# Kernel optimization log

Measured on AMD Instinct MI355X. Metric: run time of the kernel, lower is better.

Reference implementation:

```python
import jax, jax.numpy as jnp
import numpy as np

NU, NI, E, DIN, D, NB, NC = 100000, 50000, 2000000, 64, 64, 2, 5


def setup_inputs() -> dict:
    key = jax.random.key(0)
    ks = jax.random.split(key, 10)
    return {
        "ufeat": jax.random.normal(ks[0], (NU, DIN), dtype=jnp.float32),
        "ifeat": jax.random.normal(ks[1], (NI, DIN), dtype=jnp.float32),
        "c_u": jax.random.uniform(ks[2], (NU, 1), dtype=jnp.float32),
        "c_i": jax.random.uniform(ks[3], (NI, 1), dtype=jnp.float32),
        "W_user": jax.random.normal(ks[4], (DIN, D), dtype=jnp.float32) * (1.0 / np.sqrt(DIN)),
        "W_item": jax.random.normal(ks[5], (DIN, D), dtype=jnp.float32) * (1.0 / np.sqrt(DIN)),
        "P": jax.random.normal(ks[6], (NB, D, D), dtype=jnp.float32) * (1.0 / np.sqrt(D)),
        "Wc": jax.random.normal(ks[7], (NC, NB), dtype=jnp.float32),
        "src": jax.random.randint(ks[8], (E,), 0, NU, dtype=jnp.int32),
        "dst": jax.random.randint(ks[9], (E,), 0, NI, dtype=jnp.int32),
    }


def reference(ufeat, ifeat, c_u, c_i, W_user, W_item, P, Wc, src, dst):
    # --- GCMCGraphConv user->item: feat @ W, scale by c_j, copy_u + sum scatter, scale by c_i ---
    msg_u = (ufeat @ W_user) * c_u                                   # [NU, D]
    h_item = jax.ops.segment_sum(msg_u[src], dst, num_segments=ifeat.shape[0]) * c_i  # [NI, D]
    # --- GCMCGraphConv item->user (reverse edges) ---
    msg_i = (ifeat @ W_item) * c_i                                   # [NI, D]
    h_user = jax.ops.segment_sum(msg_i[dst], src, num_segments=ufeat.shape[0]) * c_u  # [NU, D]
    # --- BiDecoder: per-edge bilinear dot for each basis, then basis combine ---
    hu_b = jnp.einsum('nd,sde->nse', h_user, P)                      # [NU, NB, D]
    sr = jnp.einsum('esd,ed->es', hu_b[src], h_item[dst])            # [E, NB]
    out = sr @ Wc.T                                                  # [E, NC]
    return out
```

## Files before the change

### kernel.cpp

```cpp
#include <hip/hip_runtime.h>
#include <hip/hip_fp16.h>

#define NUu 100000
#define NIi 50000
#define NEe 2000000

#define NCBI   25
#define NCBU   49
#define NCB    74
#define NBLK1  512
#define CHUNK1 ((NEe + NBLK1 - 1) / NBLK1)

#define BR    16
#define NBKI  3125
#define NBKU  6250
#define CAPI  896
#define CAPU  512
#define FSUB2 8
#define FOWN2 16
#define FPC   128

__global__ __launch_bounds__(256) void gemm64_both(
    const float* __restrict__ ufeat, const float* __restrict__ ifeat,
    const float* __restrict__ W_user, const float* __restrict__ W_item,
    const float* __restrict__ c_u, const float* __restrict__ c_i,
    __half* __restrict__ msg_u, __half* __restrict__ msg_i)
{
    __shared__ float Wl[64 * 64];
    __shared__ float rows[16][64];
    const int tid  = threadIdx.x;
    const int user = (blockIdx.x < (NUu + 15) / 16) ? 1 : 0;
    const int bid  = user ? blockIdx.x : blockIdx.x - (NUu + 15) / 16;
    const float* feat = user ? ufeat : ifeat;
    const float* W    = user ? W_user : W_item;
    const float* cvec = user ? c_u : c_i;
    __half* out       = user ? msg_u : msg_i;
    const int N       = user ? NUu : NIi;

    for (int i = tid; i < 4096; i += 256) Wl[i] = W[i];
    const int r0 = bid * 16;
    for (int i = tid; i < 16 * 64; i += 256) {
        int r = r0 + (i >> 6);
        rows[i >> 6][i & 63] = (r < N) ? feat[(size_t)r * 64 + (i & 63)] : 0.f;
    }
    __syncthreads();
    const int col = tid & 63;
    const int rq  = tid >> 6;
    for (int rr = rq; rr < 16; rr += 4) {
        int r = r0 + rr;
        if (r >= N) continue;
        float s = 0.f;
        #pragma unroll
        for (int k = 0; k < 64; ++k)
            s = fmaf(rows[rr][k], Wl[k * 64 + col], s);
        out[(size_t)r * 64 + col] = __float2half(s * cvec[r]);
    }
}

__global__ __launch_bounds__(256) void hist1(
    const int* __restrict__ src, const int* __restrict__ dst, int* __restrict__ counts)
{
    __shared__ int cnt[NCB];
    const int tid = threadIdx.x;
    if (tid < NCB) cnt[tid] = 0;
    __syncthreads();
    const int beg = blockIdx.x * CHUNK1;
    const int end = min(NEe, beg + CHUNK1);
    for (int t = beg + tid; t < end; t += 256) {
        int s = src[t], d = dst[t];
        atomicAdd(&cnt[d >> 11], 1);
        atomicAdd(&cnt[NCBI + (s >> 11)], 1);
    }
    __syncthreads();
    if (tid < NCB) counts[tid * NBLK1 + blockIdx.x] = cnt[tid];
}

__global__ __launch_bounds__(256) void scan1(
    const int* __restrict__ counts, int* __restrict__ slotbase, int* __restrict__ rowptrC)
{
    __shared__ int tot[NCB], base[NCB];
    const int tid = threadIdx.x;
    if (tid < NCB) {
        int s = 0;
        for (int b = 0; b < NBLK1; ++b) s += counts[tid * NBLK1 + b];
        tot[tid] = s;
    }
    __syncthreads();
    if (tid == 0) {
        int run = 0;
        for (int c = 0; c < NCB; ++c) { base[c] = run; rowptrC[c] = run; run += tot[c]; }
        rowptrC[NCB] = run;
    }
    __syncthreads();
    if (tid < NCB) {
        int run = base[tid];
        for (int b = 0; b < NBLK1; ++b) {
            slotbase[tid * NBLK1 + b] = run;
            run += counts[tid * NBLK1 + b];
        }
    }
}

__global__ __launch_bounds__(256) void fill1(
    const int* __restrict__ src, const int* __restrict__ dst,
    const int* __restrict__ slotbase, unsigned int* __restrict__ payC)
{
    __shared__ int cur[NCB];
    const int tid = threadIdx.x;
    if (tid < NCB) cur[tid] = slotbase[tid * NBLK1 + blockIdx.x];
    __syncthreads();
    const int beg = blockIdx.x * CHUNK1;
    const int end = min(NEe, beg + CHUNK1);
    for (int t = beg + tid; t < end; t += 256) {
        int s = src[t], d = dst[t];
        int p1 = atomicAdd(&cur[d >> 11], 1);
        payC[p1] = ((unsigned)(d & 2047) << 17) | (unsigned)s;
        int p2 = atomicAdd(&cur[NCBI + (s >> 11)], 1);
        payC[p2] = ((unsigned)(s & 2047) << 16) | (unsigned)d;
    }
}

__global__ __launch_bounds__(256) void fine_split2(
    const unsigned int* __restrict__ payC, const int* __restrict__ rowptrC,
    unsigned int* __restrict__ payI, int* __restrict__ cntFI,
    unsigned int* __restrict__ payU, int* __restrict__ cntFU)
{
    __shared__ int cur[FOWN2];
    const int tid = threadIdx.x;
    int bid = blockIdx.x;
    const int user = (bid >= NCBI * FSUB2) ? 1 : 0;
    if (user) bid -= NCBI * FSUB2;
    const int cbl = bid / FSUB2;
    const int sub = bid % FSUB2;
    const int c   = user ? (NCBI + cbl) : cbl;
    const int CAP = user ? CAPU : CAPI;
    unsigned int* __restrict__ payF = user ? payU : payI;
    int*          __restrict__ cntF = user ? cntFU : cntFI;

    if (tid < FOWN2) cur[tid] = 0;
    __syncthreads();

    const int beg = rowptrC[c], end = rowptrC[c + 1];
    const int a    = min(end, beg + ((4 - (beg & 3)) & 3));
    const int vend = a + ((end - a) & ~3);

#define FS_PROC(u)                                                          \
    {                                                                       \
        unsigned int _u = (u);                                              \
        int lr  = user ? (int)(_u >> 16) : (int)(_u >> 17);                 \
        int fbl = lr >> 4;                                                  \
        if ((fbl >> 4) == sub) {                                            \
            int pos = atomicAdd(&cur[fbl & 15], 1);                         \
            if (pos < CAP) {                                                \
                unsigned int g = user ? (_u & 0xffffu) : (_u & 0x1ffffu);   \
                payF[(size_t)(cbl * FPC + fbl) * CAP + pos] =               \
                    ((unsigned)(lr & 15) << 17) | g;                        \
            }                                                               \
        }                                                                   \
    }

    if (tid < a - beg) FS_PROC(payC[beg + tid]);
    for (int i = a + tid * 4; i < vend; i += 1024) {
        uint4 v = *(const uint4*)(payC + i);
        FS_PROC(v.x); FS_PROC(v.y); FS_PROC(v.z); FS_PROC(v.w);
    }
    {
        int i = vend + tid;
        if (i < end) FS_PROC(payC[i]);
    }
#undef FS_PROC

    __syncthreads();
    if (tid < FOWN2)
        cntF[cbl * FPC + sub * FOWN2 + tid] = min(cur[tid], CAP);
}

__global__ __launch_bounds__(256) void seg_both(
    const unsigned int* __restrict__ payI, const int* __restrict__ cntFI,
    const __half* __restrict__ msg_u, const float* __restrict__ c_i,
    __half2* __restrict__ h_item,
    const unsigned int* __restrict__ payU, const int* __restrict__ cntFU,
    const __half* __restrict__ msg_i, const float* __restrict__ c_u,
    __half2* __restrict__ h_user)
{
    __shared__ unsigned int sorted[CAPI];
    __shared__ float acc[BR * 64];
    __shared__ int cnt16[BR];
    __shared__ int base16[BR];
    const int tid  = threadIdx.x;
    const int user = (blockIdx.x >= NBKI) ? 1 : 0;
    const int buk  = user ? (blockIdx.x - NBKI) : blockIdx.x;
    const int CAP  = user ? CAPU : CAPI;
    const int len  = min((user ? cntFU : cntFI)[buk], CAP);
    const unsigned int* bp = (user ? payU : payI) + (size_t)buk * CAP;
    const __half* msg      = user ? msg_i : msg_u;
    const float* cvec      = user ? c_u : c_i;
    __half2* hout          = user ? h_user : h_item;
    const int N            = user ? NUu : NIi;

    for (int i = tid; i < BR * 64; i += 256) acc[i] = 0.f;
    if (tid < BR) cnt16[tid] = 0;
    __syncthreads();
    for (int i = tid; i < len; i += 256)
        atomicAdd(&cnt16[bp[i] >> 17], 1);
    __syncthreads();
    if (tid == 0) {
        int run = 0;
        #pragma unroll
        for (int r = 0; r < BR; ++r) { base16[r] = run; run += cnt16[r]; }
    }
    __syncthreads();
    if (tid < BR) cnt16[tid] = base16[tid];
    __syncthreads();
    for (int i = tid; i < len; i += 256) {
        unsigned int p = bp[i];
        int pos = atomicAdd(&cnt16[p >> 17], 1);
        sorted[pos] = p;
    }
    __syncthreads();

    const int lane  = tid & 63;
    const int wv    = tid >> 6;
    const int chunk = (len + 3) >> 2;
    const int lo = wv * chunk;
    const int hi = min(lo + chunk, len);
    float facc = 0.f;
    int crow = -1;
    for (int i = lo; i < hi; i += 8) {
        unsigned int pk[8];
        float vk[8];
        #pragma unroll
        for (int k = 0; k < 8; ++k)
            pk[k] = sorted[min(i + k, hi - 1)];
        #pragma unroll
        for (int k = 0; k < 8; ++k)
            vk[k] = __half2float(msg[(size_t)(pk[k] & 0x1ffffu) * 64 + lane]);
        #pragma unroll
        for (int k = 0; k < 8; ++k) {
            if (i + k < hi) {
                int r = (int)(pk[k] >> 17);
                if (r != crow) {
                    if (crow >= 0) atomicAdd(&acc[crow * 64 + lane], facc);
                    crow = r;
                    facc = 0.f;
                }
                facc += vk[k];
            }
        }
    }
    if (crow >= 0) atomicAdd(&acc[crow * 64 + lane], facc);
    __syncthreads();

    const int r0 = buk * BR;
    for (int idx = tid; idx < BR * 32; idx += 256) {
        int r = idx >> 5, j2 = idx & 31;
        int R = r0 + r;
        if (R < N) {
            float c = cvec[R];
            hout[(size_t)R * 32 + j2] =
                __floats2half2_rn(acc[r * 64 + 2 * j2] * c, acc[r * 64 + 2 * j2 + 1] * c);
        }
    }
}

__global__ __launch_bounds__(256) void basis_projT_h(
    const __half* __restrict__ h, const float* __restrict__ P,
    __half* __restrict__ hb, int N)
{
    __shared__ float Pl[2 * 64 * 65];
    __shared__ float rows[8][64];
    const int tid = threadIdx.x;
    for (int i = tid; i < 8192; i += 256) {
        int b = i >> 12, rem = i & 4095, dg = rem >> 6, kg = rem & 63;
        Pl[b * 4160 + kg * 65 + dg] = P[i];
    }
    const int r0 = blockIdx.x * 8;
    for (int i = tid; i < 512; i += 256) {
        int r = r0 + (i >> 6);
        rows[i >> 6][i & 63] = (r < N) ? __half2float(h[(size_t)r * 64 + (i & 63)]) : 0.f;
    }
    __syncthreads();
    const int col = tid & 63;
    const int b   = (tid >> 6) & 1;
    const int rh  = tid >> 7;
    for (int rr = rh; rr < 8; rr += 2) {
        int r = r0 + rr;
        if (r >= N) continue;
        float s = 0.f;
        #pragma unroll
        for (int k = 0; k < 64; ++k)
            s = fmaf(rows[rr][k], Pl[b * 4160 + k * 65 + col], s);
        hb[((size_t)r * 2 + b) * 64 + col] = __float2half(s);
    }
}

__global__ __launch_bounds__(256) void edge_out_h(
    const uint4* __restrict__ hu,
    const uint4* __restrict__ hib,
    const int* __restrict__ src, const int* __restrict__ dst,
    const float* __restrict__ Wc, float* __restrict__ out, int nocts)
{
    const int l   = threadIdx.x & 63;
    const int q   = l >> 3;
    const int j   = l & 7;
    const int wid = blockIdx.x * 4 + (threadIdx.x >> 6);
    const int nw  = gridDim.x * 4;
    const float wcA = (j < 5) ? Wc[2 * j]     : 0.f;
    const float wcB = (j < 5) ? Wc[2 * j + 1] : 0.f;
    for (int t = wid; t < nocts; t += nw) {
        int e = t * 8 + q;
        int s = src[e], d = dst[e];
        uint4 ua = hu[(size_t)s * 8 + j];
        uint4 b0 = hib[(size_t)d * 16 + j];
        uint4 b1 = hib[(size_t)d * 16 + 8 + j];
        float2 u0 = __half22float2(*(const __half2*)&ua.x);
        float2 u1 = __half22float2(*(const __half2*)&ua.y);
        float2 u2 = __half22float2(*(const __half2*)&ua.z);
        float2 u3 = __half22float2(*(const __half2*)&ua.w);
        float2 v0 = __half22float2(*(const __half2*)&b0.x);
        float2 v1 = __half22float2(*(const __half2*)&b0.y);
        float2 v2 = __half22float2(*(const __half2*)&b0.z);
        float2 v3 = __half22float2(*(const __half2*)&b0.w);
        float2 w0 = __half22float2(*(const __half2*)&b1.x);
        float2 w1 = __half22float2(*(const __half2*)&b1.y);
        float2 w2 = __half22float2(*(const __half2*)&b1.z);
        float2 w3 = __half22float2(*(const __half2*)&b1.w);
        float p0 = u0.x * v0.x + u0.y * v0.y + u1.x * v1.x + u1.y * v1.y
                 + u2.x * v2.x + u2.y * v2.y + u3.x * v3.x + u3.y * v3.y;
        float p1 = u0.x * w0.x + u0.y * w0.y + u1.x * w1.x + u1.y * w1.y
                 + u2.x * w2.x + u2.y * w2.y + u3.x * w3.x + u3.y * w3.y;
        #pragma unroll
        for (int m = 1; m < 8; m <<= 1) {
            p0 += __shfl_xor(p0, m, 64);
            p1 += __shfl_xor(p1, m, 64);
        }
        if (j < 5) out[(size_t)e * 5 + j] = p0 * wcA + p1 * wcB;
    }
}

extern "C" void kernel_launch(void* const* d_in, const int* in_sizes, int n_in,
                              void* d_out, int out_size, void* d_ws, size_t ws_size,
                              hipStream_t stream) {
    const float* ufeat  = (const float*)d_in[0];
    const float* ifeat  = (const float*)d_in[1];
    const float* c_u    = (const float*)d_in[2];
    const float* c_i    = (const float*)d_in[3];
    const float* W_user = (const float*)d_in[4];
    const float* W_item = (const float*)d_in[5];
    const float* P      = (const float*)d_in[6];
    const float* Wc     = (const float*)d_in[7];
    const int*   src    = (const int*)d_in[8];
    const int*   dst    = (const int*)d_in[9];
    float* out = (float*)d_out;
    char*  ws  = (char*)d_ws;

    __half*       msg_u    = (__half*)(ws);
    __half*       msg_i    = (__half*)(ws + 12800000);
    __half*       h_item   = (__half*)(ws + 19200000);
    __half*       h_user   = (__half*)(ws + 25600000);
    unsigned int* payC     = (unsigned int*)(ws + 38400000);
    __half*       hi_b     = (__half*)(ws + 38400000);
    unsigned int* payI     = (unsigned int*)(ws + 54400000);
    unsigned int* payU     = (unsigned int*)(ws + 65600000);
    int*          counts   = (int*)(ws + 78400000);
    int*          slotbase = (int*)(ws + 78551552);
    int*          rowptrC  = (int*)(ws + 78703104);
    int*          cntFI    = (int*)(ws + 78703404);
    int*          cntFU    = (int*)(ws + 78716204);

    gemm64_both<<<(NUu + 15) / 16 + (NIi + 15) / 16, 256, 0, stream>>>(
        ufeat, ifeat, W_user, W_item, c_u, c_i, msg_u, msg_i);

    hist1<<<NBLK1, 256, 0, stream>>>(src, dst, counts);
    scan1<<<1, 256, 0, stream>>>(counts, slotbase, rowptrC);
    fill1<<<NBLK1, 256, 0, stream>>>(src, dst, slotbase, payC);
    fine_split2<<<(NCBI + NCBU) * FSUB2, 256, 0, stream>>>(
        payC, rowptrC, payI, cntFI, payU, cntFU);

    seg_both<<<NBKI + NBKU, 256, 0, stream>>>(
        payI, cntFI, msg_u, c_i, (__half2*)h_item,
        payU, cntFU, msg_i, c_u, (__half2*)h_user);

    basis_projT_h<<<(NIi + 7) / 8, 256, 0, stream>>>(h_item, P, hi_b, NIi);
    edge_out_h<<<2048, 256, 0, stream>>>(
        (const uint4*)h_user, (const uint4*)hi_b, src, dst, Wc, out, NEe / 8);
}
```

Baseline: 425.7 us.

## Vectorize edge binning loads and split segment gather into half2 half-waves

```diff
diff --git a/kernel.cpp b/kernel.cpp
--- a/kernel.cpp
+++ b/kernel.cpp
@@ -8,8 +8,8 @@
 #define NCBI   25
 #define NCBU   49
 #define NCB    74
-#define NBLK1  512
-#define CHUNK1 ((NEe + NBLK1 - 1) / NBLK1)
+#define NBLK1  500
+#define CHUNK1 4000
 
 #define BR    16
 #define NBKI  3125
@@ -65,11 +65,17 @@
     if (tid < NCB) cnt[tid] = 0;
     __syncthreads();
     const int beg = blockIdx.x * CHUNK1;
-    const int end = min(NEe, beg + CHUNK1);
-    for (int t = beg + tid; t < end; t += 256) {
-        int s = src[t], d = dst[t];
-        atomicAdd(&cnt[d >> 11], 1);
-        atomicAdd(&cnt[NCBI + (s >> 11)], 1);
+    for (int i = beg + tid * 4; i < beg + CHUNK1; i += 1024) {
+        uint4 s4 = *(const uint4*)(src + i);
+        uint4 d4 = *(const uint4*)(dst + i);
+        atomicAdd(&cnt[d4.x >> 11], 1);
+        atomicAdd(&cnt[d4.y >> 11], 1);
+        atomicAdd(&cnt[d4.z >> 11], 1);
+        atomicAdd(&cnt[d4.w >> 11], 1);
+        atomicAdd(&cnt[NCBI + (s4.x >> 11)], 1);
+        atomicAdd(&cnt[NCBI + (s4.y >> 11)], 1);
+        atomicAdd(&cnt[NCBI + (s4.z >> 11)], 1);
+        atomicAdd(&cnt[NCBI + (s4.w >> 11)], 1);
     }
     __syncthreads();
     if (tid < NCB) counts[tid * NBLK1 + blockIdx.x] = cnt[tid];
@@ -110,14 +116,23 @@
     if (tid < NCB) cur[tid] = slotbase[tid * NBLK1 + blockIdx.x];
     __syncthreads();
     const int beg = blockIdx.x * CHUNK1;
-    const int end = min(NEe, beg + CHUNK1);
-    for (int t = beg + tid; t < end; t += 256) {
-        int s = src[t], d = dst[t];
-        int p1 = atomicAdd(&cur[d >> 11], 1);
-        payC[p1] = ((unsigned)(d & 2047) << 17) | (unsigned)s;
-        int p2 = atomicAdd(&cur[NCBI + (s >> 11)], 1);
-        payC[p2] = ((unsigned)(s & 2047) << 16) | (unsigned)d;
-    }
+#define F1_PROC(ss, dd)                                                     \
+    {                                                                       \
+        int _s = (int)(ss), _d = (int)(dd);                                 \
+        int p1 = atomicAdd(&cur[_d >> 11], 1);                              \
+        payC[p1] = ((unsigned)(_d & 2047) << 17) | (unsigned)_s;            \
+        int p2 = atomicAdd(&cur[NCBI + (_s >> 11)], 1);                     \
+        payC[p2] = ((unsigned)(_s & 2047) << 16) | (unsigned)_d;            \
+    }
+    for (int i = beg + tid * 4; i < beg + CHUNK1; i += 1024) {
+        uint4 s4 = *(const uint4*)(src + i);
+        uint4 d4 = *(const uint4*)(dst + i);
+        F1_PROC(s4.x, d4.x);
+        F1_PROC(s4.y, d4.y);
+        F1_PROC(s4.z, d4.z);
+        F1_PROC(s4.w, d4.w);
+    }
+#undef F1_PROC
 }
 
 __global__ __launch_bounds__(256) void fine_split2(
@@ -185,70 +200,81 @@
 {
     __shared__ unsigned int sorted[CAPI];
     __shared__ float acc[BR * 64];
-    __shared__ int cnt16[BR];
-    __shared__ int base16[BR];
+    __shared__ int cnt16w[4][BR];
     const int tid  = threadIdx.x;
+    const int wv   = tid >> 6;
     const int user = (blockIdx.x >= NBKI) ? 1 : 0;
     const int buk  = user ? (blockIdx.x - NBKI) : blockIdx.x;
     const int CAP  = user ? CAPU : CAPI;
     const int len  = min((user ? cntFU : cntFI)[buk], CAP);
     const unsigned int* bp = (user ? payU : payI) + (size_t)buk * CAP;
-    const __half* msg      = user ? msg_i : msg_u;
+    const __half2* msg2    = (const __half2*)(user ? msg_i : msg_u);
     const float* cvec      = user ? c_u : c_i;
     __half2* hout          = user ? h_user : h_item;
     const int N            = user ? NUu : NIi;
 
     for (int i = tid; i < BR * 64; i += 256) acc[i] = 0.f;
-    if (tid < BR) cnt16[tid] = 0;
+    if (tid < 64) ((int*)cnt16w)[tid] = 0;
     __syncthreads();
     for (int i = tid; i < len; i += 256)
-        atomicAdd(&cnt16[bp[i] >> 17], 1);
+        atomicAdd(&cnt16w[wv][bp[i] >> 17], 1);
     __syncthreads();
     if (tid == 0) {
         int run = 0;
         #pragma unroll
-        for (int r = 0; r < BR; ++r) { base16[r] = run; run += cnt16[r]; }
-    }
-    __syncthreads();
-    if (tid < BR) cnt16[tid] = base16[tid];
+        for (int r = 0; r < BR; ++r)
+            for (int w = 0; w < 4; ++w) {
+                int cw = cnt16w[w][r];
+                cnt16w[w][r] = run;
+                run += cw;
+            }
+    }
     __syncthreads();
     for (int i = tid; i < len; i += 256) {
         unsigned int p = bp[i];
-        int pos = atomicAdd(&cnt16[p >> 17], 1);
+        int pos = atomicAdd(&cnt16w[wv][p >> 17], 1);
         sorted[pos] = p;
     }
     __syncthreads();
 
-    const int lane  = tid & 63;
-    const int wv    = tid >> 6;
-    const int chunk = (len + 3) >> 2;
-    const int lo = wv * chunk;
+    const int col2  = tid & 31;
+    const int half  = (tid >> 5) & 1;
+    const int sid   = wv * 2 + half;
+    const int chunk = (len + 7) >> 3;
+    const int lo = sid * chunk;
     const int hi = min(lo + chunk, len);
-    float facc = 0.f;
+    float2 facc = make_float2(0.f, 0.f);
     int crow = -1;
     for (int i = lo; i < hi; i += 8) {
         unsigned int pk[8];
-        float vk[8];
+        float2 vk[8];
         #pragma unroll
         for (int k = 0; k < 8; ++k)
             pk[k] = sorted[min(i + k, hi - 1)];
         #pragma unroll
         for (int k = 0; k < 8; ++k)
-            vk[k] = __half2float(msg[(size_t)(pk[k] & 0x1ffffu) * 64 + lane]);
+            vk[k] = __half22float2(msg2[(size_t)(pk[k] & 0x1ffffu) * 32 + col2]);
         #pragma unroll
         for (int k = 0; k < 8; ++k) {
             if (i + k < hi) {
                 int r = (int)(pk[k] >> 17);
                 if (r != crow) {
-                    if (crow >= 0) atomicAdd(&acc[crow * 64 + lane], facc);
+                    if (crow >= 0) {
+                        atomicAdd(&acc[crow * 64 + 2 * col2],     facc.x);
+                        atomicAdd(&acc[crow * 64 + 2 * col2 + 1], facc.y);
+                    }
                     crow = r;
-                    facc = 0.f;
+                    facc = make_float2(0.f, 0.f);
                 }
-                facc += vk[k];
+                facc.x += vk[k].x;
+                facc.y += vk[k].y;
             }
         }
     }
-    if (crow >= 0) atomicAdd(&acc[crow * 64 + lane], facc);
+    if (crow >= 0) {
+        atomicAdd(&acc[crow * 64 + 2 * col2],     facc.x);
+        atomicAdd(&acc[crow * 64 + 2 * col2 + 1], facc.y);
+    }
     __syncthreads();
 
     const int r0 = buk * BR;
```

After: 404.6 us. -5.0%, faster.
